# Kernel tuning notes

Measured on AMD Instinct MI355X. Metric: run time of the kernel, lower is better.

## Reference

```python
import jax, jax.numpy as jnp
import numpy as np

D_MODEL = 512
D_STATE = 128
D_CONV = 4
EXPAND = 2
HEADDIM = 64
NLAYERS = 2
D_INNER = EXPAND * D_MODEL          # 1024
NHEADS = D_INNER // HEADDIM         # 16
CONV_DIM = D_INNER + 2 * D_STATE    # 1280 (x, B, C share the depthwise conv)
D_IN_PROJ = 2 * D_INNER + 2 * D_STATE + NHEADS  # 2320 (z, xBC, dt)
VOCAB = 40
SEQ = 64
BATCH = 512
NUM_CLASSES = 2
FC_HID = 128
EPS = 1e-5


def setup_inputs() -> dict:
    key = jax.random.key(0)
    ks = jax.random.split(key, 12)
    x = jax.random.randint(ks[0], (BATCH, SEQ), 0, VOCAB)
    emb = jax.random.uniform(ks[1], (VOCAB, D_MODEL), minval=-0.1, maxval=0.1)
    emb = emb.at[0].set(0.0)  # padding_idx=0
    pos = jax.random.normal(ks[2], (1, SEQ, D_MODEL)) * 0.02
    in_proj_w = jax.random.normal(ks[3], (NLAYERS, D_IN_PROJ, D_MODEL)) * 0.02
    conv_w = jax.random.normal(ks[4], (NLAYERS, CONV_DIM, D_CONV)) * 0.1
    conv_b = jnp.zeros((NLAYERS, CONV_DIM))
    dt0 = jax.random.uniform(ks[5], (NLAYERS, NHEADS), minval=1e-3, maxval=0.1)
    dt_bias = dt0 + jnp.log(-jnp.expm1(-dt0))  # inverse softplus of dt0
    A_log = jnp.log(jax.random.uniform(ks[6], (NLAYERS, NHEADS), minval=1.0, maxval=16.0))
    D_skip = jnp.ones((NLAYERS, NHEADS))
    norm_w = jnp.ones((NLAYERS, D_INNER))
    out_proj_w = jax.random.normal(ks[7], (NLAYERS, D_MODEL, D_INNER)) * 0.02
    ln_g = jnp.ones((NLAYERS, D_MODEL))
    ln_b = jnp.zeros((NLAYERS, D_MODEL))
    fc1_w = jax.random.uniform(ks[8], (FC_HID, D_MODEL), minval=-0.1, maxval=0.1)
    fc1_b = jnp.zeros((FC_HID,))
    fc2_w = jax.random.uniform(ks[9], (NUM_CLASSES, FC_HID), minval=-0.1, maxval=0.1)
    fc2_b = jnp.zeros((NUM_CLASSES,))
    return dict(x=x, emb=emb, pos=pos, in_proj_w=in_proj_w, conv_w=conv_w,
                conv_b=conv_b, dt_bias=dt_bias, A_log=A_log, D_skip=D_skip,
                norm_w=norm_w, out_proj_w=out_proj_w, ln_g=ln_g, ln_b=ln_b,
                fc1_w=fc1_w, fc1_b=fc1_b, fc2_w=fc2_w, fc2_b=fc2_b)


def _layernorm(h, g, b):
    mu = jnp.mean(h, axis=-1, keepdims=True)
    var = jnp.mean(jnp.square(h - mu), axis=-1, keepdims=True)
    return (h - mu) * jax.lax.rsqrt(var + EPS) * g + b


def _mamba2_block(h, in_proj_w, conv_w, conv_b, dt_bias, A_log, D_skip, norm_w, out_proj_w):
    b, s, _ = h.shape
    zxbcdt = jnp.einsum('bsd,ed->bse', h, in_proj_w)  # [b,s,D_IN_PROJ]
    z = zxbcdt[..., :D_INNER]
    xBC = zxbcdt[..., D_INNER:D_INNER + CONV_DIM]
    dt_raw = zxbcdt[..., D_INNER + CONV_DIM:]          # [b,s,NHEADS]
    # causal depthwise 1D conv + silu
    xBC_t = jnp.pad(jnp.swapaxes(xBC, 1, 2), ((0, 0), (0, 0), (D_CONV - 1, 0)))
    conv = jax.lax.conv_general_dilated(xBC_t, conv_w[:, None, :], (1,), 'VALID',
                                        feature_group_count=CONV_DIM)
    xBC = jax.nn.silu(jnp.swapaxes(conv + conv_b[None, :, None], 1, 2))
    xs = xBC[..., :D_INNER].reshape(b, s, NHEADS, HEADDIM)
    Bm = xBC[..., D_INNER:D_INNER + D_STATE]           # [b,s,n] (ngroups=1)
    Cm = xBC[..., D_INNER + D_STATE:]                  # [b,s,n]
    dt = jax.nn.softplus(dt_raw + dt_bias)             # [b,s,h]
    A = -jnp.exp(A_log)                                # [h], negative
    # exact quadratic (1-semiseparable) SSD form, equal to the selective scan
    cum = jnp.cumsum(dt * A, axis=1)                   # [b,s,h]
    diff = cum[:, :, None, :] - cum[:, None, :, :]     # [b,i,j,h] <= 0 for i>=j
    causal = jnp.tril(jnp.ones((s, s), dtype=bool))
    L = jnp.exp(jnp.where(causal[None, :, :, None], diff, -jnp.inf))  # decay mask
    scores = jnp.einsum('bin,bjn->bij', Cm, Bm)
    M = scores[..., None] * L                          # [b,i,j,h]
    y = jnp.einsum('bijh,bjh,bjhp->bihp', M, dt, xs)
    y = y + D_skip[None, None, :, None] * xs
    y = y.reshape(b, s, D_INNER)
    # gated RMSNorm
    y = y * jax.nn.silu(z)
    y = y * jax.lax.rsqrt(jnp.mean(jnp.square(y), axis=-1, keepdims=True) + EPS) * norm_w
    return jnp.einsum('bsi,di->bsd', y, out_proj_w)


def reference(x, emb, pos, in_proj_w, conv_w, conv_b, dt_bias, A_log, D_skip,
              norm_w, out_proj_w, ln_g, ln_b, fc1_w, fc1_b, fc2_w, fc2_b):
    h = emb[x] + pos[:, :x.shape[1], :]  # dropout is identity in eval
    for l in range(NLAYERS):
        y = _mamba2_block(h, in_proj_w[l], conv_w[l], conv_b[l], dt_bias[l],
                          A_log[l], D_skip[l], norm_w[l], out_proj_w[l])
        h = h + _layernorm(y, ln_g[l], ln_b[l])
    pm = (jnp.sum(h, axis=-1) != 0).astype(h.dtype)[..., None]  # [b,s,1]
    pooled = jnp.sum(h * pm, axis=1) / jnp.clip(jnp.sum(pm, axis=1), 1.0, None)
    hid = jax.nn.relu(pooled @ fc1_w.T + fc1_b)
    return hid @ fc2_w.T + fc2_b
```

## Files before the change

kernel.cpp:

```cpp
#include <hip/hip_runtime.h>
#include <hip/hip_bf16.h>

#define D_MODEL   512
#define D_STATE   128
#define D_CONV    4
#define HEADDIM   64
#define NLAYERS   2
#define D_INNER   1024
#define NHEADS    16
#define CONV_DIM  1280
#define D_IN_PROJ 2320
#define NPAD      2432
#define SEQ       64
#define BATCH     512
#define NTOK      (BATCH*SEQ)
#define FC_HID    128
#define EPS       1e-5f

using bf16 = __hip_bfloat16;
typedef __bf16 bf16x8 __attribute__((ext_vector_type(8)));
typedef float  f32x4  __attribute__((ext_vector_type(4)));

__device__ __forceinline__ float b2f(bf16 v)  { return __bfloat162float(v); }
__device__ __forceinline__ bf16  f2b(float v) { return __float2bfloat16(v); }
__device__ __forceinline__ float bflo(unsigned u){ return __builtin_bit_cast(float, u << 16); }
__device__ __forceinline__ float bfhi(unsigned u){ return __builtin_bit_cast(float, u & 0xffff0000u); }

__device__ __forceinline__ void gl_lds16(const void* g, void* l) {
    __builtin_amdgcn_global_load_lds((const __attribute__((address_space(1))) void*)g,
                                     (__attribute__((address_space(3))) void*)l, 16, 0, 0);
}

__global__ __launch_bounds__(256) void k_embed(const int* __restrict__ x,
        const float* __restrict__ emb, const float* __restrict__ pos,
        float* __restrict__ h, bf16* __restrict__ hb) {
    int idx = blockIdx.x*256 + threadIdx.x;
    int d   = idx & (D_MODEL-1);
    int tok = idx >> 9;
    int s   = tok & (SEQ-1);
    int v   = x[tok];
    float r = emb[v*D_MODEL + d] + pos[s*D_MODEL + d];
    h[idx]  = r;
    hb[idx] = f2b(r);
}

__global__ __launch_bounds__(256) void k_cvtw(const float* __restrict__ src,
        bf16* __restrict__ dst, int R, int Kc, int total8) {
    int idx = blockIdx.x*256 + threadIdx.x;
    if (idx >= total8) return;
    int e0 = idx*8;
    int r = e0 / Kc, c = e0 % Kc;
    bf16 tb[8];
    if (r < R) {
        float4 f0 = *(const float4*)(src + (size_t)r*Kc + c);
        float4 f1 = *(const float4*)(src + (size_t)r*Kc + c + 4);
        tb[0]=f2b(f0.x); tb[1]=f2b(f0.y); tb[2]=f2b(f0.z); tb[3]=f2b(f0.w);
        tb[4]=f2b(f1.x); tb[5]=f2b(f1.y); tb[6]=f2b(f1.z); tb[7]=f2b(f1.w);
    } else {
        #pragma unroll
        for (int e=0;e<8;e++) tb[e] = f2b(0.f);
    }
    *(uint4*)(dst + (size_t)r*Kc + c) = *(uint4*)&tb[0];
}

template<int FUSE, int KDIM>
__global__ __launch_bounds__(256) void k_gemm128(const bf16* __restrict__ A,
        const bf16* __restrict__ B, bf16* __restrict__ C,
        bf16* __restrict__ xbcc, float* __restrict__ dt, float* __restrict__ cum,
        const float* __restrict__ cw, const float* __restrict__ cb,
        const float* __restrict__ dt_bias, const float* __restrict__ A_log,
        int Nout, int nbx, int ctok)
{
    constexpr int NT = KDIM / 64;
    __shared__ __align__(16) char lds[65536];
    bf16* Cs = (bf16*)lds;

    const int nwg = gridDim.x;
    const int q = nwg >> 3, r = nwg & 7;
    const int xcd = blockIdx.x & 7, loc = blockIdx.x >> 3;
    const int wg = ((xcd < r) ? xcd*(q+1) : r*(q+1) + (xcd-r)*q) + loc;
    const int m0 = (wg / nbx) * 128;
    const int n0 = (wg % nbx) * 128;

    const int t = threadIdx.x;
    const int wid = t >> 6, lane = t & 63;
    const int lr = lane & 15, lg = lane >> 4;
    const int wm = (wid >> 1)*64, wn = (wid & 1)*64;
    const int srow = wid*32;
    const int sr   = lane >> 3;
    const int scol = ((lane & 7) ^ sr) * 8;

    const bf16* Abase = A + (size_t)(m0 + srow + sr)*KDIM + scol;
    const bf16* Bbase = B + (size_t)(n0 + srow + sr)*KDIM + scol;

    f32x4 acc[4][4] = {};
    char* bc = lds;
    char* bn = lds + 32768;

    auto STAGE = [&](char* buf, int kk) {
        #pragma unroll
        for (int c = 0; c < 4; c++) {
            gl_lds16(Abase + (size_t)(c*8)*KDIM + kk, buf + (srow + c*8)*128);
            gl_lds16(Bbase + (size_t)(c*8)*KDIM + kk, buf + 16384 + (srow + c*8)*128);
        }
    };

    STAGE(bc, 0);
    asm volatile("s_waitcnt vmcnt(0)" ::: "memory");
    __builtin_amdgcn_s_barrier();

    #pragma unroll
    for (int kt = 0; kt < NT; kt++) {
        if (kt + 1 < NT) STAGE(bn, (kt+1)*64);
        #pragma unroll
        for (int ks = 0; ks < 64; ks += 32) {
            bf16x8 a[4], b[4];
            #pragma unroll
            for (int mi=0;mi<4;mi++) {
                int ra = wm + mi*16 + lr;
                a[mi] = *(const bf16x8*)(bc + ra*128 + ((((ks>>3)+lg) ^ (ra&7))<<4));
            }
            #pragma unroll
            for (int ni=0;ni<4;ni++) {
                int rb = wn + ni*16 + lr;
                b[ni] = *(const bf16x8*)(bc + 16384 + rb*128 + ((((ks>>3)+lg) ^ (rb&7))<<4));
            }
            __builtin_amdgcn_s_setprio(1);
            #pragma unroll
            for (int mi=0;mi<4;mi++)
                #pragma unroll
                for (int ni=0;ni<4;ni++)
                    acc[mi][ni] = __builtin_amdgcn_mfma_f32_16x16x32_bf16(a[mi], b[ni], acc[mi][ni], 0,0,0);
            __builtin_amdgcn_s_setprio(0);
        }
        asm volatile("s_waitcnt vmcnt(0)" ::: "memory");
        __builtin_amdgcn_s_barrier();
        char* tb2 = bc; bc = bn; bn = tb2;
    }
    __builtin_amdgcn_sched_barrier(0);

    #pragma unroll
    for (int mi=0;mi<4;mi++)
        #pragma unroll
        for (int ni=0;ni<4;ni++)
            #pragma unroll
            for (int rr=0;rr<4;rr++)
                Cs[(wm+mi*16+lg*4+rr)*136 + wn+ni*16+lr] = f2b(acc[mi][ni][rr]);
    __syncthreads();

    const int rsub = t >> 4;
    const int c8   = (t & 15) * 8;

    if (FUSE == 0 || n0 < 1024) {
        const int strd = (FUSE == 0) ? Nout : 1024;
        #pragma unroll
        for (int it = 0; it < 8; it++) {
            int row = it*16 + rsub;
            int gcol = n0 + c8;
            if (FUSE == 0 && gcol >= Nout) continue;
            *(uint4*)(C + (size_t)(m0+row)*strd + gcol) = *(const uint4*)&Cs[row*136 + c8];
        }
    } else if (n0 < 2304) {
        const int cbase = n0 - 1024 + c8;
        float4 wreg[8]; float bias[8];
        #pragma unroll
        for (int e=0;e<8;e++) wreg[e] = *(const float4*)(cw + (size_t)(cbase+e)*4);
        {
            float4 b0 = *(const float4*)(cb + cbase);
            float4 b1 = *(const float4*)(cb + cbase + 4);
            bias[0]=b0.x; bias[1]=b0.y; bias[2]=b0.z; bias[3]=b0.w;
            bias[4]=b1.x; bias[5]=b1.y; bias[6]=b1.z; bias[7]=b1.w;
        }
        #pragma unroll
        for (int it = 0; it < 8; it++) {
            int row = it*16 + rsub;
            int sl  = row & (SEQ-1);
            float m3 = (sl >= 3) ? 1.f : 0.f;
            float m2 = (sl >= 2) ? 1.f : 0.f;
            float m1 = (sl >= 1) ? 1.f : 0.f;
            const bf16* sm3 = &Cs[(row-3)*136 + c8];
            const bf16* sm2 = &Cs[(row-2)*136 + c8];
            const bf16* sm1 = &Cs[(row-1)*136 + c8];
            const bf16* sm0 = &Cs[(row  )*136 + c8];
            float a[8];
            #pragma unroll
            for (int e=0;e<8;e++) {
                a[e] = bias[e]
                     + m3 * b2f(sm3[e]) * wreg[e].x
                     + m2 * b2f(sm2[e]) * wreg[e].y
                     + m1 * b2f(sm1[e]) * wreg[e].z
                     +      b2f(sm0[e]) * wreg[e].w;
            }
            bf16 outv[8];
            #pragma unroll
            for (int e=0;e<8;e++) outv[e] = f2b(a[e] / (1.f + __expf(-a[e])));
            *(uint4*)(xbcc + (size_t)(m0+row)*CONV_DIM + cbase) = *(uint4*)&outv[0];
        }
    } else {
        for (int p = wid; p < 32; p += 4) {
            int sq = p >> 4, head = p & 15;
            float raw = b2f(Cs[(sq*64 + lane)*136 + head]) + dt_bias[head];
            float dval = (raw > 20.f) ? raw : log1pf(__expf(raw));
            float Ah = -__expf(A_log[head]);
            float cc = dval * Ah;
            #pragma unroll
            for (int o=1;o<64;o<<=1) { float v = __shfl_up(cc, o); if (lane >= o) cc += v; }
            int tok = m0 + sq*64 + lane;
            dt [(size_t)head*ctok + tok] = dval;
            cum[(size_t)head*ctok + tok] = cc;
        }
    }
}

__global__ __launch_bounds__(256) void k_ssd(const bf16* __restrict__ xbcc,
        const float* __restrict__ dt, const float* __restrict__ cum,
        const float* __restrict__ Dskip, bf16* __restrict__ y, int ctok) {
    __shared__ float scores[64][66];
    __shared__ __align__(16) bf16 Wb [64][72];
    __shared__ __align__(16) bf16 xsT[64][72];
    __shared__ __align__(16) bf16 ys [64][72];
    const int bid = blockIdx.x;
    const int b   = bid >> 1;
    const int hg  = (bid & 1) * 8;
    const int t = threadIdx.x;
    const size_t tokbase = (size_t)b*SEQ;
    const int lane = t & 63, lr = lane & 15, lg = lane >> 4;
    const int w = t >> 6;

    {
        int i0 = w*16;
        f32x4 sacc[4] = {};
        const bf16* Cbase = xbcc + tokbase*CONV_DIM + D_INNER + D_STATE;
        const bf16* Bbase = xbcc + tokbase*CONV_DIM + D_INNER;
        #pragma unroll
        for (int ks = 0; ks < D_STATE; ks += 32) {
            bf16x8 af = *(const bf16x8*)(Cbase + (size_t)(i0+lr)*CONV_DIM + ks + lg*8);
            #pragma unroll
            for (int jt = 0; jt < 4; jt++) {
                bf16x8 bfr = *(const bf16x8*)(Bbase + (size_t)(jt*16+lr)*CONV_DIM + ks + lg*8);
                sacc[jt] = __builtin_amdgcn_mfma_f32_16x16x32_bf16(af, bfr, sacc[jt], 0,0,0);
            }
        }
        #pragma unroll
        for (int jt=0;jt<4;jt++)
            #pragma unroll
            for (int rr=0;rr<4;rr++)
                scores[i0 + lg*4 + rr][jt*16 + lr] = sacc[jt][rr];
    }

    const int wi = t >> 2;
    const int wj0 = (t & 3) * 16;

    for (int hl = 0; hl < 8; hl++) {
        const int hh = hg + hl;
        const size_t cbase = (size_t)hh*ctok + tokbase;
        __syncthreads();

        #pragma unroll
        for (int cc = 0; cc < 2; cc++) {
            int ch = cc*256 + t;
            int rr = ch >> 3, c8 = (ch & 7)*8;
            uint4 v = *(const uint4*)(xbcc + (tokbase + rr)*CONV_DIM + hh*HEADDIM + c8);
            const bf16* pv = (const bf16*)&v;
            #pragma unroll
            for (int e=0;e<8;e++) xsT[c8+e][rr] = pv[e];
        }
        {
            float cum_i = cum[cbase + wi];
            float cjf[16], djf[16];
            #pragma unroll
            for (int qq=0; qq<4; qq++) {
                float4 a4 = *(const float4*)(cum + cbase + wj0 + qq*4);
                float4 d4 = *(const float4*)(dt  + cbase + wj0 + qq*4);
                cjf[qq*4+0]=a4.x; cjf[qq*4+1]=a4.y; cjf[qq*4+2]=a4.z; cjf[qq*4+3]=a4.w;
                djf[qq*4+0]=d4.x; djf[qq*4+1]=d4.y; djf[qq*4+2]=d4.z; djf[qq*4+3]=d4.w;
            }
            bf16 tb[16];
            #pragma unroll
            for (int e=0;e<16;e++) {
                int j = wj0 + e;
                float wv = (j <= wi) ? scores[wi][j] * __expf(cum_i - cjf[e]) * djf[e] : 0.f;
                tb[e] = f2b(wv);
            }
            *(uint4*)&Wb[wi][wj0]   = *(uint4*)&tb[0];
            *(uint4*)&Wb[wi][wj0+8] = *(uint4*)&tb[8];
        }
        __syncthreads();

        {
            float dsk = Dskip[hh];
            f32x4 yacc[4] = {};
            #pragma unroll
            for (int ks = 0; ks < 64; ks += 32) {
                bf16x8 a = *(const bf16x8*)&Wb[w*16 + lr][ks + lg*8];
                #pragma unroll
                for (int n=0; n<4; n++) {
                    bf16x8 bb = *(const bf16x8*)&xsT[n*16 + lr][ks + lg*8];
                    yacc[n] = __builtin_amdgcn_mfma_f32_16x16x32_bf16(a, bb, yacc[n], 0,0,0);
                }
            }
            #pragma unroll
            for (int n=0; n<4; n++)
                #pragma unroll
                for (int rr=0; rr<4; rr++) {
                    int row = w*16 + lg*4 + rr;
                    int col = n*16 + lr;
                    ys[row][col] = f2b(yacc[n][rr] + dsk * b2f(xsT[col][row]));
                }
        }
        __syncthreads();

        #pragma unroll
        for (int cc = 0; cc < 2; cc++) {
            int ch = cc*256 + t;
            int rr = ch >> 3, c8 = (ch & 7)*8;
            *(uint4*)(y + (tokbase + rr)*D_INNER + hh*HEADDIM + c8) = *(const uint4*)&ys[rr][c8];
        }
    }
}

__global__ __launch_bounds__(256) void k_gaterms(bf16* __restrict__ y,
        const bf16* __restrict__ zbuf, const float* __restrict__ nw) {
    int tok = blockIdx.x, t = threadIdx.x;
    __shared__ float red[4];
    int d = t*4;
    uint2 yv = *(const uint2*)(y    + (size_t)tok*D_INNER + d);
    uint2 zv = *(const uint2*)(zbuf + (size_t)tok*D_INNER + d);
    const unsigned* yu = (const unsigned*)&yv;
    const unsigned* zu = (const unsigned*)&zv;
    float g[4]; float ss = 0.f;
    #pragma unroll
    for (int e=0;e<2;e++) {
        float y0 = bflo(yu[e]), y1 = bfhi(yu[e]);
        float z0 = bflo(zu[e]), z1 = bfhi(zu[e]);
        float g0 = y0 * z0 / (1.f + __expf(-z0));
        float g1 = y1 * z1 / (1.f + __expf(-z1));
        g[2*e] = g0; g[2*e+1] = g1;
        ss += g0*g0 + g1*g1;
    }
    for (int o=32;o>0;o>>=1) ss += __shfl_down(ss, o);
    if ((t & 63) == 0) red[t>>6] = ss;
    __syncthreads();
    float tot = red[0]+red[1]+red[2]+red[3];
    float scale = rsqrtf(tot/(float)D_INNER + EPS);
    bf16 outv[4];
    #pragma unroll
    for (int e=0;e<4;e++) outv[e] = f2b(g[e] * scale * nw[d+e]);
    *(uint2*)(y + (size_t)tok*D_INNER + d) = *(uint2*)&outv[0];
}

__global__ __launch_bounds__(256) void k_resln(float* __restrict__ h,
        bf16* __restrict__ hb, const bf16* __restrict__ tmp,
        const float* __restrict__ g, const float* __restrict__ bb) {
    int tok = blockIdx.x, t = threadIdx.x;
    __shared__ float redS[4], redQ[4];
    int d = t*2;
    unsigned u = *(const unsigned*)(tmp + (size_t)tok*D_MODEL + d);
    float v0 = bflo(u), v1 = bfhi(u);
    float s = v0+v1, q = v0*v0+v1*v1;
    for (int o=32;o>0;o>>=1){ s += __shfl_down(s,o); q += __shfl_down(q,o); }
    if ((t&63)==0){ redS[t>>6]=s; redQ[t>>6]=q; }
    __syncthreads();
    float S = redS[0]+redS[1]+redS[2]+redS[3];
    float Q = redQ[0]+redQ[1]+redQ[2]+redQ[3];
    float mu  = S/(float)D_MODEL;
    float var = Q/(float)D_MODEL - mu*mu;
    float inv = rsqrtf(var + EPS);
    size_t base = (size_t)tok*D_MODEL + d;
    float h0 = h[base]   + (v0-mu)*inv*g[d]   + bb[d];
    float h1 = h[base+1] + (v1-mu)*inv*g[d+1] + bb[d+1];
    h[base] = h0; h[base+1] = h1;
    bf16 o2[2] = { f2b(h0), f2b(h1) };
    *(unsigned*)(hb + base) = *(unsigned*)&o2[0];
}

__global__ __launch_bounds__(256) void k_pool(const float* __restrict__ h,
        float* __restrict__ pooled) {
    int b = blockIdx.x, t = threadIdx.x;
    __shared__ float ps[64][4];
    __shared__ float pm[64];
    __shared__ float cntS;
    {
        int s = t >> 2, q = t & 3;
        const float4* row = (const float4*)(h + ((size_t)b*SEQ + s)*D_MODEL + q*128);
        float acc = 0;
        #pragma unroll 8
        for (int e=0;e<32;e++) { float4 f = row[e]; acc += f.x+f.y+f.z+f.w; }
        ps[s][q] = acc;
    }
    __syncthreads();
    if (t < 64) pm[t] = (ps[t][0]+ps[t][1]+ps[t][2]+ps[t][3]) != 0.f ? 1.f : 0.f;
    __syncthreads();
    if (t == 0) { float c=0; for (int s2=0;s2<64;s2++) c+=pm[s2]; cntS = fmaxf(c,1.f); }
    __syncthreads();
    float cnt = cntS;
    #pragma unroll
    for (int rep=0;rep<2;rep++) {
        int d = t + rep*256;
        float acc = 0;
        for (int s2=0;s2<64;s2++) acc += h[((size_t)b*SEQ+s2)*D_MODEL + d] * pm[s2];
        pooled[(size_t)b*D_MODEL + d] = acc / cnt;
    }
}

__global__ __launch_bounds__(128) void k_fc(const float* __restrict__ pooled,
        const float* __restrict__ w1, const float* __restrict__ b1,
        const float* __restrict__ w2, const float* __restrict__ b2,
        float* __restrict__ out) {
    int b = blockIdx.x, j = threadIdx.x;
    __shared__ float hid[FC_HID];
    const float* p  = pooled + (size_t)b*D_MODEL;
    const float* wr = w1 + (size_t)j*D_MODEL;
    float acc = b1[j];
    for (int d=0; d<D_MODEL; d+=4)
        acc += p[d]*wr[d] + p[d+1]*wr[d+1] + p[d+2]*wr[d+2] + p[d+3]*wr[d+3];
    hid[j] = fmaxf(acc, 0.f);
    __syncthreads();
    if (j < 2) {
        float o = b2[j];
        for (int k=0;k<FC_HID;k++) o += hid[k]*w2[j*FC_HID+k];
        out[b*2 + j] = o;
    }
}

extern "C" void kernel_launch(void* const* d_in, const int* in_sizes, int n_in,
                              void* d_out, int out_size, void* d_ws, size_t ws_size,
                              hipStream_t stream) {
    (void)in_sizes; (void)n_in; (void)out_size;
    const int*   x        = (const int*)  d_in[0];
    const float* emb      = (const float*)d_in[1];
    const float* pos      = (const float*)d_in[2];
    const float* in_proj  = (const float*)d_in[3];
    const float* conv_w   = (const float*)d_in[4];
    const float* conv_b   = (const float*)d_in[5];
    const float* dt_bias  = (const float*)d_in[6];
    const float* A_log    = (const float*)d_in[7];
    const float* D_skip   = (const float*)d_in[8];
    const float* norm_w   = (const float*)d_in[9];
    const float* out_proj = (const float*)d_in[10];
    const float* ln_g     = (const float*)d_in[11];
    const float* ln_b     = (const float*)d_in[12];
    const float* fc1_w    = (const float*)d_in[13];
    const float* fc1_b    = (const float*)d_in[14];
    const float* fc2_w    = (const float*)d_in[15];
    const float* fc2_b    = (const float*)d_in[16];
    float* out = (float*)d_out;

    const size_t H_B   = (size_t)NTOK * D_MODEL * 4;
    const size_t HB_B  = (size_t)NTOK * D_MODEL * 2;
    const size_t WPI_B = (size_t)NPAD * D_MODEL * 2;
    const size_t WPO_B = (size_t)D_MODEL * D_INNER * 2;
    const size_t PBASE = H_B + HB_B + NLAYERS*(WPI_B + WPO_B);

    const size_t PER_TOK = 2048 + 2560 + 2048 + 128;
    int CB = BATCH;
    while (CB > 8 && PBASE + (size_t)CB*SEQ*PER_TOK > ws_size) CB >>= 1;
    const int CT = CB * SEQ;
    const int NC = BATCH / CB;

    char* ws = (char*)d_ws;
    float* h    = (float*)(ws);
    bf16*  hb   = (bf16*) (ws + H_B);
    bf16*  wpi  = (bf16*) (ws + H_B + HB_B);
    bf16*  wpo  = (bf16*) (ws + H_B + HB_B + NLAYERS*WPI_B);
    char*  tr   = ws + PBASE;
    bf16*  zbuf = (bf16*) (tr);
    bf16*  xbcc = (bf16*) (tr + (size_t)CT*2048);
    bf16*  ybuf = (bf16*) (tr + (size_t)CT*(2048+2560));
    float* dt   = (float*)(tr + (size_t)CT*(2048+2560+2048));
    float* cum  = dt + (size_t)CT*NHEADS;
    bf16*  tmp  = xbcc;
    float* pooled = (float*)tr;

    for (int l = 0; l < NLAYERS; l++) {
        int t8i = NPAD*D_MODEL/8;
        k_cvtw<<<(t8i+255)/256, 256, 0, stream>>>(in_proj + (size_t)l*D_IN_PROJ*D_MODEL,
                wpi + (size_t)l*NPAD*D_MODEL, D_IN_PROJ, D_MODEL, t8i);
        int t8o = D_MODEL*D_INNER/8;
        k_cvtw<<<(t8o+255)/256, 256, 0, stream>>>(out_proj + (size_t)l*D_MODEL*D_INNER,
                wpo + (size_t)l*D_MODEL*D_INNER, D_MODEL, D_INNER, t8o);
    }

    k_embed<<<(NTOK*D_MODEL)/256, 256, 0, stream>>>(x, emb, pos, h, hb);

    const int NBX_I = NPAD/128;
    const int NBX_O = D_MODEL/128;

    for (int l = 0; l < NLAYERS; l++) {
        const bf16* wi = wpi + (size_t)l*NPAD*D_MODEL;
        const bf16* wo = wpo + (size_t)l*D_MODEL*D_INNER;
        for (int c = 0; c < NC; c++) {
            const int tok0 = c * CT;
            float* hc  = h  + (size_t)tok0 * D_MODEL;
            bf16*  hbc = hb + (size_t)tok0 * D_MODEL;
            k_gemm128<1,512><<<(CT/128)*NBX_I, 256, 0, stream>>>(hbc, wi, zbuf,
                    xbcc, dt, cum,
                    conv_w + (size_t)l*CONV_DIM*D_CONV, conv_b + (size_t)l*CONV_DIM,
                    dt_bias + l*NHEADS, A_log + l*NHEADS,
                    NPAD, NBX_I, CT);
            k_ssd<<<CB*2, 256, 0, stream>>>(xbcc, dt, cum, D_skip + l*NHEADS, ybuf, CT);
            k_gaterms<<<CT, 256, 0, stream>>>(ybuf, zbuf, norm_w + (size_t)l*D_INNER);
            k_gemm128<0,1024><<<(CT/128)*NBX_O, 256, 0, stream>>>(ybuf, wo, tmp,
                    nullptr, nullptr, nullptr, nullptr, nullptr, nullptr, nullptr,
                    D_MODEL, NBX_O, CT);
            k_resln<<<CT, 256, 0, stream>>>(hc, hbc, tmp, ln_g + l*D_MODEL, ln_b + l*D_MODEL);
        }
    }

    k_pool<<<BATCH, 256, 0, stream>>>(h, pooled);
    k_fc<<<BATCH, FC_HID, 0, stream>>>(pooled, fc1_w, fc1_b, fc2_w, fc2_b, out);
}
```

Baseline: 667.2 us.

## Use 256x256 in-projection GEMM tile and vectorize elementwise kernels

Replaces the fused in-projection GEMM with a 256x256-tile, 512-thread kernel that uses 128KB of dynamic LDS and pads N to 2560. The fused conv/SiLU and dt/cumsum epilogue now runs in two 128-row halves. The embed, gated-RMSNorm and residual-LayerNorm kernels are widened to handle more elements per thread and two tokens per block. This aims to raise MFMA data reuse and cut per-block overhead, at the cost of more padded columns, lower occupancy from the large LDS footprint and higher register pressure.

```diff
diff --git a/kernel.cpp b/kernel.cpp
--- a/kernel.cpp
+++ b/kernel.cpp
@@ -10,7 +10,7 @@
 #define NHEADS    16
 #define CONV_DIM  1280
 #define D_IN_PROJ 2320
-#define NPAD      2432
+#define NPAD      2560
 #define SEQ       64
 #define BATCH     512
 #define NTOK      (BATCH*SEQ)
@@ -35,13 +35,16 @@
         const float* __restrict__ emb, const float* __restrict__ pos,
         float* __restrict__ h, bf16* __restrict__ hb) {
     int idx = blockIdx.x*256 + threadIdx.x;
-    int d   = idx & (D_MODEL-1);
-    int tok = idx >> 9;
+    int d   = (idx & 127) * 4;
+    int tok = idx >> 7;
     int s   = tok & (SEQ-1);
     int v   = x[tok];
-    float r = emb[v*D_MODEL + d] + pos[s*D_MODEL + d];
-    h[idx]  = r;
-    hb[idx] = f2b(r);
+    float4 e4 = *(const float4*)(emb + (size_t)v*D_MODEL + d);
+    float4 p4 = *(const float4*)(pos + (size_t)s*D_MODEL + d);
+    float4 r; r.x=e4.x+p4.x; r.y=e4.y+p4.y; r.z=e4.z+p4.z; r.w=e4.w+p4.w;
+    *(float4*)(h + (size_t)tok*D_MODEL + d) = r;
+    bf16 o[4] = { f2b(r.x), f2b(r.y), f2b(r.z), f2b(r.w) };
+    *(uint2*)(hb + (size_t)tok*D_MODEL + d) = *(uint2*)&o[0];
 }
 
 __global__ __launch_bounds__(256) void k_cvtw(const float* __restrict__ src,
@@ -63,15 +66,162 @@
     *(uint4*)(dst + (size_t)r*Kc + c) = *(uint4*)&tb[0];
 }
 
-template<int FUSE, int KDIM>
-__global__ __launch_bounds__(256) void k_gemm128(const bf16* __restrict__ A,
-        const bf16* __restrict__ B, bf16* __restrict__ C,
+__global__ __launch_bounds__(512) void k_gemm256(const bf16* __restrict__ A,
+        const bf16* __restrict__ B, bf16* __restrict__ zbuf,
         bf16* __restrict__ xbcc, float* __restrict__ dt, float* __restrict__ cum,
         const float* __restrict__ cw, const float* __restrict__ cb,
         const float* __restrict__ dt_bias, const float* __restrict__ A_log,
-        int Nout, int nbx, int ctok)
+        int ctok)
 {
-    constexpr int NT = KDIM / 64;
+    constexpr int KDIM = 512, NT = KDIM/64, NBX = NPAD/256;
+    extern __shared__ __align__(16) char lds[];
+    bf16* Cs = (bf16*)lds;
+
+    const int nwg = gridDim.x;
+    const int q = nwg >> 3, r = nwg & 7;
+    const int xcd = blockIdx.x & 7, loc = blockIdx.x >> 3;
+    const int wg = ((xcd < r) ? xcd*(q+1) : r*(q+1) + (xcd-r)*q) + loc;
+    const int m0 = (wg / NBX) * 256;
+    const int n0 = (wg % NBX) * 256;
+
+    const int t = threadIdx.x;
+    const int wid = t >> 6, lane = t & 63;
+    const int lr = lane & 15, lg = lane >> 4;
+    const int wm = (wid >> 2)*128, wn = (wid & 3)*64;
+    const int srow = wid*32;
+    const int sr   = lane >> 3;
+    const int scol = ((lane & 7) ^ sr) * 8;
+
+    const bf16* Abase = A + (size_t)(m0 + srow + sr)*KDIM + scol;
+    const bf16* Bbase = B + (size_t)(n0 + srow + sr)*KDIM + scol;
+
+    f32x4 acc[8][4] = {};
+    char* bc = lds;
+    char* bn = lds + 65536;
+
+    auto STAGE = [&](char* buf, int kk) {
+        #pragma unroll
+        for (int c = 0; c < 4; c++) {
+            gl_lds16(Abase + (size_t)(c*8)*KDIM + kk, buf + (srow + c*8)*128);
+            gl_lds16(Bbase + (size_t)(c*8)*KDIM + kk, buf + 32768 + (srow + c*8)*128);
+        }
+    };
+
+    STAGE(bc, 0);
+    asm volatile("s_waitcnt vmcnt(0)" ::: "memory");
+    __builtin_amdgcn_s_barrier();
+
+    #pragma unroll
+    for (int kt = 0; kt < NT; kt++) {
+        if (kt + 1 < NT) STAGE(bn, (kt+1)*64);
+        #pragma unroll
+        for (int ks = 0; ks < 64; ks += 32) {
+            bf16x8 a[8], b[4];
+            #pragma unroll
+            for (int mi=0;mi<8;mi++) {
+                int ra = wm + mi*16 + lr;
+                a[mi] = *(const bf16x8*)(bc + ra*128 + ((((ks>>3)+lg) ^ (ra&7))<<4));
+            }
+            #pragma unroll
+            for (int ni=0;ni<4;ni++) {
+                int rb = wn + ni*16 + lr;
+                b[ni] = *(const bf16x8*)(bc + 32768 + rb*128 + ((((ks>>3)+lg) ^ (rb&7))<<4));
+            }
+            __builtin_amdgcn_s_setprio(1);
+            #pragma unroll
+            for (int mi=0;mi<8;mi++)
+                #pragma unroll
+                for (int ni=0;ni<4;ni++)
+                    acc[mi][ni] = __builtin_amdgcn_mfma_f32_16x16x32_bf16(a[mi], b[ni], acc[mi][ni], 0,0,0);
+            __builtin_amdgcn_s_setprio(0);
+        }
+        asm volatile("s_waitcnt vmcnt(0)" ::: "memory");
+        __builtin_amdgcn_s_barrier();
+        char* tb2 = bc; bc = bn; bn = tb2;
+    }
+    __builtin_amdgcn_sched_barrier(0);
+
+    const int myhalf = wid >> 2;
+    const int rsub = t >> 5;
+    const int c8   = (t & 31) * 8;
+
+    for (int hp = 0; hp < 2; hp++) {
+        __syncthreads();
+        if (myhalf == hp) {
+            #pragma unroll
+            for (int mi=0;mi<8;mi++)
+                #pragma unroll
+                for (int ni=0;ni<4;ni++)
+                    #pragma unroll
+                    for (int rr=0;rr<4;rr++)
+                        Cs[(mi*16+lg*4+rr)*264 + wn+ni*16+lr] = f2b(acc[mi][ni][rr]);
+        }
+        __syncthreads();
+        const int R0 = hp*128;
+
+        if (n0 < 1024) {
+            #pragma unroll
+            for (int it = 0; it < 8; it++) {
+                int row = it*16 + rsub;
+                *(uint4*)(zbuf + (size_t)(m0+R0+row)*1024 + n0 + c8) = *(const uint4*)&Cs[row*264 + c8];
+            }
+        } else if (n0 < 2304) {
+            const int cbase = n0 - 1024 + c8;
+            float4 wreg[8]; float bias[8];
+            #pragma unroll
+            for (int e=0;e<8;e++) wreg[e] = *(const float4*)(cw + (size_t)(cbase+e)*4);
+            {
+                float4 b0 = *(const float4*)(cb + cbase);
+                float4 b1 = *(const float4*)(cb + cbase + 4);
+                bias[0]=b0.x; bias[1]=b0.y; bias[2]=b0.z; bias[3]=b0.w;
+                bias[4]=b1.x; bias[5]=b1.y; bias[6]=b1.z; bias[7]=b1.w;
+            }
+            #pragma unroll
+            for (int it = 0; it < 8; it++) {
+                int row = it*16 + rsub;
+                int sl  = row & (SEQ-1);
+                float m3 = (sl >= 3) ? 1.f : 0.f;
+                float m2 = (sl >= 2) ? 1.f : 0.f;
+                float m1 = (sl >= 1) ? 1.f : 0.f;
+                const bf16* sm3 = &Cs[(row-3)*264 + c8];
+                const bf16* sm2 = &Cs[(row-2)*264 + c8];
+                const bf16* sm1 = &Cs[(row-1)*264 + c8];
+                const bf16* sm0 = &Cs[(row  )*264 + c8];
+                float a[8];
+                #pragma unroll
+                for (int e=0;e<8;e++) {
+                    a[e] = bias[e]
+                         + m3 * b2f(sm3[e]) * wreg[e].x
+                         + m2 * b2f(sm2[e]) * wreg[e].y
+                         + m1 * b2f(sm1[e]) * wreg[e].z
+                         +      b2f(sm0[e]) * wreg[e].w;
+                }
+                bf16 outv[8];
+                #pragma unroll
+                for (int e=0;e<8;e++) outv[e] = f2b(a[e] / (1.f + __expf(-a[e])));
+                *(uint4*)(xbcc + (size_t)(m0+R0+row)*CONV_DIM + cbase) = *(uint4*)&outv[0];
+            }
+        } else {
+            for (int p = wid; p < 32; p += 8) {
+                int sq = p >> 4, head = p & 15;
+                float raw = b2f(Cs[(sq*64 + lane)*264 + head]) + dt_bias[head];
+                float dval = (raw > 20.f) ? raw : log1pf(__expf(raw));
+                float Ah = -__expf(A_log[head]);
+                float cc = dval * Ah;
+                #pragma unroll
+                for (int o=1;o<64;o<<=1) { float v = __shfl_up(cc, o); if (lane >= o) cc += v; }
+                int tok = m0 + R0 + sq*64 + lane;
+                dt [(size_t)head*ctok + tok] = dval;
+                cum[(size_t)head*ctok + tok] = cc;
+            }
+        }
+    }
+}
+
+__global__ __launch_bounds__(256) void k_gemm128(const bf16* __restrict__ A,
+        const bf16* __restrict__ B, bf16* __restrict__ C, int Nout, int nbx)
+{
+    constexpr int KDIM = 1024, NT = KDIM/64;
     __shared__ __align__(16) char lds[65536];
     bf16* Cs = (bf16*)lds;
 
@@ -147,68 +297,12 @@
             for (int rr=0;rr<4;rr++)
                 Cs[(wm+mi*16+lg*4+rr)*136 + wn+ni*16+lr] = f2b(acc[mi][ni][rr]);
     __syncthreads();
-
     const int rsub = t >> 4;
     const int c8   = (t & 15) * 8;
-
-    if (FUSE == 0 || n0 < 1024) {
-        const int strd = (FUSE == 0) ? Nout : 1024;
-        #pragma unroll
-        for (int it = 0; it < 8; it++) {
-            int row = it*16 + rsub;
-            int gcol = n0 + c8;
-            if (FUSE == 0 && gcol >= Nout) continue;
-            *(uint4*)(C + (size_t)(m0+row)*strd + gcol) = *(const uint4*)&Cs[row*136 + c8];
-        }
-    } else if (n0 < 2304) {
-        const int cbase = n0 - 1024 + c8;
-        float4 wreg[8]; float bias[8];
-        #pragma unroll
-        for (int e=0;e<8;e++) wreg[e] = *(const float4*)(cw + (size_t)(cbase+e)*4);
-        {
-            float4 b0 = *(const float4*)(cb + cbase);
-            float4 b1 = *(const float4*)(cb + cbase + 4);
-            bias[0]=b0.x; bias[1]=b0.y; bias[2]=b0.z; bias[3]=b0.w;
-            bias[4]=b1.x; bias[5]=b1.y; bias[6]=b1.z; bias[7]=b1.w;
-        }
-        #pragma unroll
-        for (int it = 0; it < 8; it++) {
-            int row = it*16 + rsub;
-            int sl  = row & (SEQ-1);
-            float m3 = (sl >= 3) ? 1.f : 0.f;
-            float m2 = (sl >= 2) ? 1.f : 0.f;
-            float m1 = (sl >= 1) ? 1.f : 0.f;
-            const bf16* sm3 = &Cs[(row-3)*136 + c8];
-            const bf16* sm2 = &Cs[(row-2)*136 + c8];
-            const bf16* sm1 = &Cs[(row-1)*136 + c8];
-            const bf16* sm0 = &Cs[(row  )*136 + c8];
-            float a[8];
-            #pragma unroll
-            for (int e=0;e<8;e++) {
-                a[e] = bias[e]
-                     + m3 * b2f(sm3[e]) * wreg[e].x
-                     + m2 * b2f(sm2[e]) * wreg[e].y
-                     + m1 * b2f(sm1[e]) * wreg[e].z
-                     +      b2f(sm0[e]) * wreg[e].w;
-            }
-            bf16 outv[8];
-            #pragma unroll
-            for (int e=0;e<8;e++) outv[e] = f2b(a[e] / (1.f + __expf(-a[e])));
-            *(uint4*)(xbcc + (size_t)(m0+row)*CONV_DIM + cbase) = *(uint4*)&outv[0];
-        }
-    } else {
-        for (int p = wid; p < 32; p += 4) {
-            int sq = p >> 4, head = p & 15;
-            float raw = b2f(Cs[(sq*64 + lane)*136 + head]) + dt_bias[head];
-            float dval = (raw > 20.f) ? raw : log1pf(__expf(raw));
-            float Ah = -__expf(A_log[head]);
-            float cc = dval * Ah;
-            #pragma unroll
-            for (int o=1;o<64;o<<=1) { float v = __shfl_up(cc, o); if (lane >= o) cc += v; }
-            int tok = m0 + sq*64 + lane;
-            dt [(size_t)head*ctok + tok] = dval;
-            cum[(size_t)head*ctok + tok] = cc;
-        }
+    #pragma unroll
+    for (int it = 0; it < 8; it++) {
+        int row = it*16 + rsub;
+        *(uint4*)(C + (size_t)(m0+row)*Nout + n0 + c8) = *(const uint4*)&Cs[row*136 + c8];
     }
 }
 
@@ -321,16 +415,18 @@
 
 __global__ __launch_bounds__(256) void k_gaterms(bf16* __restrict__ y,
         const bf16* __restrict__ zbuf, const float* __restrict__ nw) {
-    int tok = blockIdx.x, t = threadIdx.x;
-    __shared__ float red[4];
-    int d = t*4;
-    uint2 yv = *(const uint2*)(y    + (size_t)tok*D_INNER + d);
-    uint2 zv = *(const uint2*)(zbuf + (size_t)tok*D_INNER + d);
+    int tok = blockIdx.x*2 + (threadIdx.x >> 7);
+    int t   = threadIdx.x & 127;
+    int hi  = threadIdx.x >> 7, wv = (threadIdx.x >> 6) & 1;
+    __shared__ float red[2][2];
+    int d = t*8;
+    uint4 yv = *(const uint4*)(y    + (size_t)tok*D_INNER + d);
+    uint4 zv = *(const uint4*)(zbuf + (size_t)tok*D_INNER + d);
     const unsigned* yu = (const unsigned*)&yv;
     const unsigned* zu = (const unsigned*)&zv;
-    float g[4]; float ss = 0.f;
+    float g[8]; float ss = 0.f;
     #pragma unroll
-    for (int e=0;e<2;e++) {
+    for (int e=0;e<4;e++) {
         float y0 = bflo(yu[e]), y1 = bfhi(yu[e]);
         float z0 = bflo(zu[e]), z1 = bfhi(zu[e]);
         float g0 = y0 * z0 / (1.f + __expf(-z0));
@@ -339,39 +435,47 @@
         ss += g0*g0 + g1*g1;
     }
     for (int o=32;o>0;o>>=1) ss += __shfl_down(ss, o);
-    if ((t & 63) == 0) red[t>>6] = ss;
+    if ((threadIdx.x & 63) == 0) red[hi][wv] = ss;
     __syncthreads();
-    float tot = red[0]+red[1]+red[2]+red[3];
-    float scale = rsqrtf(tot/(float)D_INNER + EPS);
-    bf16 outv[4];
+    float scale = rsqrtf((red[hi][0]+red[hi][1])/(float)D_INNER + EPS);
+    bf16 outv[8];
     #pragma unroll
-    for (int e=0;e<4;e++) outv[e] = f2b(g[e] * scale * nw[d+e]);
-    *(uint2*)(y + (size_t)tok*D_INNER + d) = *(uint2*)&outv[0];
+    for (int e=0;e<8;e++) outv[e] = f2b(g[e] * scale * nw[d+e]);
+    *(uint4*)(y + (size_t)tok*D_INNER + d) = *(uint4*)&outv[0];
 }
 
 __global__ __launch_bounds__(256) void k_resln(float* __restrict__ h,
         bf16* __restrict__ hb, const bf16* __restrict__ tmp,
         const float* __restrict__ g, const float* __restrict__ bb) {
-    int tok = blockIdx.x, t = threadIdx.x;
-    __shared__ float redS[4], redQ[4];
-    int d = t*2;
-    unsigned u = *(const unsigned*)(tmp + (size_t)tok*D_MODEL + d);
-    float v0 = bflo(u), v1 = bfhi(u);
-    float s = v0+v1, q = v0*v0+v1*v1;
-    for (int o=32;o>0;o>>=1){ s += __shfl_down(s,o); q += __shfl_down(q,o); }
-    if ((t&63)==0){ redS[t>>6]=s; redQ[t>>6]=q; }
+    int tok = blockIdx.x*2 + (threadIdx.x >> 7);
+    int t   = threadIdx.x & 127;
+    int hi  = threadIdx.x >> 7, wv = (threadIdx.x >> 6) & 1;
+    __shared__ float redS[2][2], redQ[2][2];
+    int d = t*4;
+    uint2 u2 = *(const uint2*)(tmp + (size_t)tok*D_MODEL + d);
+    const unsigned* uu = (const unsigned*)&u2;
+    float v0 = bflo(uu[0]), v1 = bfhi(uu[0]), v2 = bflo(uu[1]), v3 = bfhi(uu[1]);
+    float s = v0+v1+v2+v3;
+    float qq = v0*v0+v1*v1+v2*v2+v3*v3;
+    for (int o=32;o>0;o>>=1){ s += __shfl_down(s,o); qq += __shfl_down(qq,o); }
+    if ((threadIdx.x & 63) == 0){ redS[hi][wv]=s; redQ[hi][wv]=qq; }
     __syncthreads();
-    float S = redS[0]+redS[1]+redS[2]+redS[3];
-    float Q = redQ[0]+redQ[1]+redQ[2]+redQ[3];
+    float S = redS[hi][0]+redS[hi][1];
+    float Q = redQ[hi][0]+redQ[hi][1];
     float mu  = S/(float)D_MODEL;
     float var = Q/(float)D_MODEL - mu*mu;
     float inv = rsqrtf(var + EPS);
     size_t base = (size_t)tok*D_MODEL + d;
-    float h0 = h[base]   + (v0-mu)*inv*g[d]   + bb[d];
-    float h1 = h[base+1] + (v1-mu)*inv*g[d+1] + bb[d+1];
-    h[base] = h0; h[base+1] = h1;
-    bf16 o2[2] = { f2b(h0), f2b(h1) };
-    *(unsigned*)(hb + base) = *(unsigned*)&o2[0];
+    float4 h4 = *(const float4*)(h + base);
+    float4 g4 = *(const float4*)(g + d);
+    float4 b4 = *(const float4*)(bb + d);
+    h4.x += (v0-mu)*inv*g4.x + b4.x;
+    h4.y += (v1-mu)*inv*g4.y + b4.y;
+    h4.z += (v2-mu)*inv*g4.z + b4.z;
+    h4.w += (v3-mu)*inv*g4.w + b4.w;
+    *(float4*)(h + base) = h4;
+    bf16 o4[4] = { f2b(h4.x), f2b(h4.y), f2b(h4.z), f2b(h4.w) };
+    *(uint2*)(hb + base) = *(uint2*)&o4[0];
 }
 
 __global__ __launch_bounds__(256) void k_pool(const float* __restrict__ h,
@@ -381,12 +485,12 @@
     __shared__ float pm[64];
     __shared__ float cntS;
     {
-        int s = t >> 2, q = t & 3;
-        const float4* row = (const float4*)(h + ((size_t)b*SEQ + s)*D_MODEL + q*128);
+        int s = t >> 2, qq = t & 3;
+        const float4* row = (const float4*)(h + ((size_t)b*SEQ + s)*D_MODEL + qq*128);
         float acc = 0;
         #pragma unroll 8
         for (int e=0;e<32;e++) { float4 f = row[e]; acc += f.x+f.y+f.z+f.w; }
-        ps[s][q] = acc;
+        ps[s][qq] = acc;
     }
     __syncthreads();
     if (t < 64) pm[t] = (ps[t][0]+ps[t][1]+ps[t][2]+ps[t][3]) != 0.f ? 1.f : 0.f;
@@ -446,6 +550,9 @@
     const float* fc2_b    = (const float*)d_in[16];
     float* out = (float*)d_out;
 
+    (void)hipFuncSetAttribute((const void*)k_gemm256,
+            hipFuncAttributeMaxDynamicSharedMemorySize, 131072);
+
     const size_t H_B   = (size_t)NTOK * D_MODEL * 4;
     const size_t HB_B  = (size_t)NTOK * D_MODEL * 2;
     const size_t WPI_B = (size_t)NPAD * D_MODEL * 2;
@@ -481,9 +588,8 @@
                 wpo + (size_t)l*D_MODEL*D_INNER, D_MODEL, D_INNER, t8o);
     }
 
-    k_embed<<<(NTOK*D_MODEL)/256, 256, 0, stream>>>(x, emb, pos, h, hb);
-
-    const int NBX_I = NPAD/128;
+    k_embed<<<(NTOK*128)/256, 256, 0, stream>>>(x, emb, pos, h, hb);
+
     const int NBX_O = D_MODEL/128;
 
     for (int l = 0; l < NLAYERS; l++) {
@@ -493,17 +599,14 @@
             const int tok0 = c * CT;
             float* hc  = h  + (size_t)tok0 * D_MODEL;
             bf16*  hbc = hb + (size_t)tok0 * D_MODEL;
-            k_gemm128<1,512><<<(CT/128)*NBX_I, 256, 0, stream>>>(hbc, wi, zbuf,
+            k_gemm256<<<(CT/256)*(NPAD/256), 512, 131072, stream>>>(hbc, wi, zbuf,
                     xbcc, dt, cum,
                     conv_w + (size_t)l*CONV_DIM*D_CONV, conv_b + (size_t)l*CONV_DIM,
-                    dt_bias + l*NHEADS, A_log + l*NHEADS,
-                    NPAD, NBX_I, CT);
+                    dt_bias + l*NHEADS, A_log + l*NHEADS, CT);
             k_ssd<<<CB*2, 256, 0, stream>>>(xbcc, dt, cum, D_skip + l*NHEADS, ybuf, CT);
-            k_gaterms<<<CT, 256, 0, stream>>>(ybuf, zbuf, norm_w + (size_t)l*D_INNER);
-            k_gemm128<0,1024><<<(CT/128)*NBX_O, 256, 0, stream>>>(ybuf, wo, tmp,
-                    nullptr, nullptr, nullptr, nullptr, nullptr, nullptr, nullptr,
-                    D_MODEL, NBX_O, CT);
-            k_resln<<<CT, 256, 0, stream>>>(hc, hbc, tmp, ln_g + l*D_MODEL, ln_b + l*D_MODEL);
+            k_gaterms<<<CT/2, 256, 0, stream>>>(ybuf, zbuf, norm_w + (size_t)l*D_INNER);
+            k_gemm128<<<(CT/128)*NBX_O, 256, 0, stream>>>(ybuf, wo, tmp, D_MODEL, NBX_O);
+            k_resln<<<CT/2, 256, 0, stream>>>(hc, hbc, tmp, ln_g + l*D_MODEL, ln_b + l*D_MODEL);
         }
     }
 
```

Result: slower. 808.2 us (+21.1%).

## Single-buffer GEMM LDS with swizzled epilogue and vectorize elementwise kernels

Applied to the files above, without the earlier changes.

The GEMM drops its double-buffered LDS prefetch for a single 32KB buffer with plain __syncthreads, which halves LDS use and may allow more resident workgroups. The output staging tile moves from padded rows to an XOR-swizzled layout. The embed, gated RMSNorm and residual LayerNorm kernels are widened to 16-byte/float4 accesses, and the norm kernels now process two tokens per block. The single-buffer GEMM loses the overlap of global loads with MFMA compute and the priority hints, so it risks more stalls.

```diff
diff --git a/kernel.cpp b/kernel.cpp
--- a/kernel.cpp
+++ b/kernel.cpp
@@ -35,13 +35,16 @@
         const float* __restrict__ emb, const float* __restrict__ pos,
         float* __restrict__ h, bf16* __restrict__ hb) {
     int idx = blockIdx.x*256 + threadIdx.x;
-    int d   = idx & (D_MODEL-1);
-    int tok = idx >> 9;
+    int d   = (idx & 127) * 4;
+    int tok = idx >> 7;
     int s   = tok & (SEQ-1);
     int v   = x[tok];
-    float r = emb[v*D_MODEL + d] + pos[s*D_MODEL + d];
-    h[idx]  = r;
-    hb[idx] = f2b(r);
+    float4 e4 = *(const float4*)(emb + (size_t)v*D_MODEL + d);
+    float4 p4 = *(const float4*)(pos + (size_t)s*D_MODEL + d);
+    float4 r; r.x=e4.x+p4.x; r.y=e4.y+p4.y; r.z=e4.z+p4.z; r.w=e4.w+p4.w;
+    *(float4*)(h + (size_t)tok*D_MODEL + d) = r;
+    bf16 o[4] = { f2b(r.x), f2b(r.y), f2b(r.z), f2b(r.w) };
+    *(uint2*)(hb + (size_t)tok*D_MODEL + d) = *(uint2*)&o[0];
 }
 
 __global__ __launch_bounds__(256) void k_cvtw(const float* __restrict__ src,
@@ -72,7 +75,7 @@
         int Nout, int nbx, int ctok)
 {
     constexpr int NT = KDIM / 64;
-    __shared__ __align__(16) char lds[65536];
+    __shared__ __align__(16) char lds[32768];
     bf16* Cs = (bf16*)lds;
 
     const int nwg = gridDim.x;
@@ -94,58 +97,47 @@
     const bf16* Bbase = B + (size_t)(n0 + srow + sr)*KDIM + scol;
 
     f32x4 acc[4][4] = {};
-    char* bc = lds;
-    char* bn = lds + 32768;
-
-    auto STAGE = [&](char* buf, int kk) {
+
+    for (int kt = 0; kt < NT; kt++) {
+        const int kk = kt*64;
         #pragma unroll
         for (int c = 0; c < 4; c++) {
-            gl_lds16(Abase + (size_t)(c*8)*KDIM + kk, buf + (srow + c*8)*128);
-            gl_lds16(Bbase + (size_t)(c*8)*KDIM + kk, buf + 16384 + (srow + c*8)*128);
-        }
-    };
-
-    STAGE(bc, 0);
-    asm volatile("s_waitcnt vmcnt(0)" ::: "memory");
-    __builtin_amdgcn_s_barrier();
-
-    #pragma unroll
-    for (int kt = 0; kt < NT; kt++) {
-        if (kt + 1 < NT) STAGE(bn, (kt+1)*64);
+            gl_lds16(Abase + (size_t)(c*8)*KDIM + kk, lds + (srow + c*8)*128);
+            gl_lds16(Bbase + (size_t)(c*8)*KDIM + kk, lds + 16384 + (srow + c*8)*128);
+        }
+        __syncthreads();
         #pragma unroll
         for (int ks = 0; ks < 64; ks += 32) {
             bf16x8 a[4], b[4];
             #pragma unroll
             for (int mi=0;mi<4;mi++) {
                 int ra = wm + mi*16 + lr;
-                a[mi] = *(const bf16x8*)(bc + ra*128 + ((((ks>>3)+lg) ^ (ra&7))<<4));
+                a[mi] = *(const bf16x8*)(lds + ra*128 + ((((ks>>3)+lg) ^ (ra&7))<<4));
             }
             #pragma unroll
             for (int ni=0;ni<4;ni++) {
                 int rb = wn + ni*16 + lr;
-                b[ni] = *(const bf16x8*)(bc + 16384 + rb*128 + ((((ks>>3)+lg) ^ (rb&7))<<4));
-            }
-            __builtin_amdgcn_s_setprio(1);
+                b[ni] = *(const bf16x8*)(lds + 16384 + rb*128 + ((((ks>>3)+lg) ^ (rb&7))<<4));
+            }
             #pragma unroll
             for (int mi=0;mi<4;mi++)
                 #pragma unroll
                 for (int ni=0;ni<4;ni++)
                     acc[mi][ni] = __builtin_amdgcn_mfma_f32_16x16x32_bf16(a[mi], b[ni], acc[mi][ni], 0,0,0);
-            __builtin_amdgcn_s_setprio(0);
-        }
-        asm volatile("s_waitcnt vmcnt(0)" ::: "memory");
-        __builtin_amdgcn_s_barrier();
-        char* tb2 = bc; bc = bn; bn = tb2;
-    }
-    __builtin_amdgcn_sched_barrier(0);
+        }
+        __syncthreads();
+    }
 
     #pragma unroll
     for (int mi=0;mi<4;mi++)
         #pragma unroll
         for (int ni=0;ni<4;ni++)
             #pragma unroll
-            for (int rr=0;rr<4;rr++)
-                Cs[(wm+mi*16+lg*4+rr)*136 + wn+ni*16+lr] = f2b(acc[mi][ni][rr]);
+            for (int rr=0;rr<4;rr++) {
+                int row = wm + mi*16 + lg*4 + rr;
+                int col = (wn + ni*16 + lr) ^ ((row & 7) << 3);
+                Cs[row*128 + col] = f2b(acc[mi][ni][rr]);
+            }
     __syncthreads();
 
     const int rsub = t >> 4;
@@ -156,9 +148,8 @@
         #pragma unroll
         for (int it = 0; it < 8; it++) {
             int row = it*16 + rsub;
-            int gcol = n0 + c8;
-            if (FUSE == 0 && gcol >= Nout) continue;
-            *(uint4*)(C + (size_t)(m0+row)*strd + gcol) = *(const uint4*)&Cs[row*136 + c8];
+            const bf16* src = &Cs[row*128 + (c8 ^ ((row & 7) << 3))];
+            *(uint4*)(C + (size_t)(m0+row)*strd + n0 + c8) = *(const uint4*)src;
         }
     } else if (n0 < 2304) {
         const int cbase = n0 - 1024 + c8;
@@ -178,10 +169,10 @@
             float m3 = (sl >= 3) ? 1.f : 0.f;
             float m2 = (sl >= 2) ? 1.f : 0.f;
             float m1 = (sl >= 1) ? 1.f : 0.f;
-            const bf16* sm3 = &Cs[(row-3)*136 + c8];
-            const bf16* sm2 = &Cs[(row-2)*136 + c8];
-            const bf16* sm1 = &Cs[(row-1)*136 + c8];
-            const bf16* sm0 = &Cs[(row  )*136 + c8];
+            const bf16* sm3 = &Cs[(row-3)*128 + (c8 ^ (((row-3) & 7) << 3))];
+            const bf16* sm2 = &Cs[(row-2)*128 + (c8 ^ (((row-2) & 7) << 3))];
+            const bf16* sm1 = &Cs[(row-1)*128 + (c8 ^ (((row-1) & 7) << 3))];
+            const bf16* sm0 = &Cs[(row  )*128 + (c8 ^ (((row  ) & 7) << 3))];
             float a[8];
             #pragma unroll
             for (int e=0;e<8;e++) {
@@ -199,13 +190,14 @@
     } else {
         for (int p = wid; p < 32; p += 4) {
             int sq = p >> 4, head = p & 15;
-            float raw = b2f(Cs[(sq*64 + lane)*136 + head]) + dt_bias[head];
+            int row = sq*64 + lane;
+            float raw = b2f(Cs[row*128 + (head ^ ((row & 7) << 3))]) + dt_bias[head];
             float dval = (raw > 20.f) ? raw : log1pf(__expf(raw));
             float Ah = -__expf(A_log[head]);
             float cc = dval * Ah;
             #pragma unroll
             for (int o=1;o<64;o<<=1) { float v = __shfl_up(cc, o); if (lane >= o) cc += v; }
-            int tok = m0 + sq*64 + lane;
+            int tok = m0 + row;
             dt [(size_t)head*ctok + tok] = dval;
             cum[(size_t)head*ctok + tok] = cc;
         }
@@ -321,16 +313,18 @@
 
 __global__ __launch_bounds__(256) void k_gaterms(bf16* __restrict__ y,
         const bf16* __restrict__ zbuf, const float* __restrict__ nw) {
-    int tok = blockIdx.x, t = threadIdx.x;
-    __shared__ float red[4];
-    int d = t*4;
-    uint2 yv = *(const uint2*)(y    + (size_t)tok*D_INNER + d);
-    uint2 zv = *(const uint2*)(zbuf + (size_t)tok*D_INNER + d);
+    int tok = blockIdx.x*2 + (threadIdx.x >> 7);
+    int t   = threadIdx.x & 127;
+    int hi  = threadIdx.x >> 7, wv = (threadIdx.x >> 6) & 1;
+    __shared__ float red[2][2];
+    int d = t*8;
+    uint4 yv = *(const uint4*)(y    + (size_t)tok*D_INNER + d);
+    uint4 zv = *(const uint4*)(zbuf + (size_t)tok*D_INNER + d);
     const unsigned* yu = (const unsigned*)&yv;
     const unsigned* zu = (const unsigned*)&zv;
-    float g[4]; float ss = 0.f;
+    float g[8]; float ss = 0.f;
     #pragma unroll
-    for (int e=0;e<2;e++) {
+    for (int e=0;e<4;e++) {
         float y0 = bflo(yu[e]), y1 = bfhi(yu[e]);
         float z0 = bflo(zu[e]), z1 = bfhi(zu[e]);
         float g0 = y0 * z0 / (1.f + __expf(-z0));
@@ -339,39 +333,47 @@
         ss += g0*g0 + g1*g1;
     }
     for (int o=32;o>0;o>>=1) ss += __shfl_down(ss, o);
-    if ((t & 63) == 0) red[t>>6] = ss;
-    __syncthreads();
-    float tot = red[0]+red[1]+red[2]+red[3];
-    float scale = rsqrtf(tot/(float)D_INNER + EPS);
-    bf16 outv[4];
+    if ((threadIdx.x & 63) == 0) red[hi][wv] = ss;
+    __syncthreads();
+    float scale = rsqrtf((red[hi][0]+red[hi][1])/(float)D_INNER + EPS);
+    bf16 outv[8];
     #pragma unroll
-    for (int e=0;e<4;e++) outv[e] = f2b(g[e] * scale * nw[d+e]);
-    *(uint2*)(y + (size_t)tok*D_INNER + d) = *(uint2*)&outv[0];
+    for (int e=0;e<8;e++) outv[e] = f2b(g[e] * scale * nw[d+e]);
+    *(uint4*)(y + (size_t)tok*D_INNER + d) = *(uint4*)&outv[0];
 }
 
 __global__ __launch_bounds__(256) void k_resln(float* __restrict__ h,
         bf16* __restrict__ hb, const bf16* __restrict__ tmp,
         const float* __restrict__ g, const float* __restrict__ bb) {
-    int tok = blockIdx.x, t = threadIdx.x;
-    __shared__ float redS[4], redQ[4];
-    int d = t*2;
-    unsigned u = *(const unsigned*)(tmp + (size_t)tok*D_MODEL + d);
-    float v0 = bflo(u), v1 = bfhi(u);
-    float s = v0+v1, q = v0*v0+v1*v1;
-    for (int o=32;o>0;o>>=1){ s += __shfl_down(s,o); q += __shfl_down(q,o); }
-    if ((t&63)==0){ redS[t>>6]=s; redQ[t>>6]=q; }
-    __syncthreads();
-    float S = redS[0]+redS[1]+redS[2]+redS[3];
-    float Q = redQ[0]+redQ[1]+redQ[2]+redQ[3];
+    int tok = blockIdx.x*2 + (threadIdx.x >> 7);
+    int t   = threadIdx.x & 127;
+    int hi  = threadIdx.x >> 7, wv = (threadIdx.x >> 6) & 1;
+    __shared__ float redS[2][2], redQ[2][2];
+    int d = t*4;
+    uint2 u2 = *(const uint2*)(tmp + (size_t)tok*D_MODEL + d);
+    const unsigned* uu = (const unsigned*)&u2;
+    float v0 = bflo(uu[0]), v1 = bfhi(uu[0]), v2 = bflo(uu[1]), v3 = bfhi(uu[1]);
+    float s = v0+v1+v2+v3;
+    float qq = v0*v0+v1*v1+v2*v2+v3*v3;
+    for (int o=32;o>0;o>>=1){ s += __shfl_down(s,o); qq += __shfl_down(qq,o); }
+    if ((threadIdx.x & 63) == 0){ redS[hi][wv]=s; redQ[hi][wv]=qq; }
+    __syncthreads();
+    float S = redS[hi][0]+redS[hi][1];
+    float Q = redQ[hi][0]+redQ[hi][1];
     float mu  = S/(float)D_MODEL;
     float var = Q/(float)D_MODEL - mu*mu;
     float inv = rsqrtf(var + EPS);
     size_t base = (size_t)tok*D_MODEL + d;
-    float h0 = h[base]   + (v0-mu)*inv*g[d]   + bb[d];
-    float h1 = h[base+1] + (v1-mu)*inv*g[d+1] + bb[d+1];
-    h[base] = h0; h[base+1] = h1;
-    bf16 o2[2] = { f2b(h0), f2b(h1) };
-    *(unsigned*)(hb + base) = *(unsigned*)&o2[0];
+    float4 h4 = *(const float4*)(h + base);
+    float4 g4 = *(const float4*)(g + d);
+    float4 b4 = *(const float4*)(bb + d);
+    h4.x += (v0-mu)*inv*g4.x + b4.x;
+    h4.y += (v1-mu)*inv*g4.y + b4.y;
+    h4.z += (v2-mu)*inv*g4.z + b4.z;
+    h4.w += (v3-mu)*inv*g4.w + b4.w;
+    *(float4*)(h + base) = h4;
+    bf16 o4[4] = { f2b(h4.x), f2b(h4.y), f2b(h4.z), f2b(h4.w) };
+    *(uint2*)(hb + base) = *(uint2*)&o4[0];
 }
 
 __global__ __launch_bounds__(256) void k_pool(const float* __restrict__ h,
@@ -381,12 +383,12 @@
     __shared__ float pm[64];
     __shared__ float cntS;
     {
-        int s = t >> 2, q = t & 3;
-        const float4* row = (const float4*)(h + ((size_t)b*SEQ + s)*D_MODEL + q*128);
+        int s = t >> 2, qq = t & 3;
+        const float4* row = (const float4*)(h + ((size_t)b*SEQ + s)*D_MODEL + qq*128);
         float acc = 0;
         #pragma unroll 8
         for (int e=0;e<32;e++) { float4 f = row[e]; acc += f.x+f.y+f.z+f.w; }
-        ps[s][q] = acc;
+        ps[s][qq] = acc;
     }
     __syncthreads();
     if (t < 64) pm[t] = (ps[t][0]+ps[t][1]+ps[t][2]+ps[t][3]) != 0.f ? 1.f : 0.f;
@@ -481,7 +483,7 @@
                 wpo + (size_t)l*D_MODEL*D_INNER, D_MODEL, D_INNER, t8o);
     }
 
-    k_embed<<<(NTOK*D_MODEL)/256, 256, 0, stream>>>(x, emb, pos, h, hb);
+    k_embed<<<(NTOK*128)/256, 256, 0, stream>>>(x, emb, pos, h, hb);
 
     const int NBX_I = NPAD/128;
     const int NBX_O = D_MODEL/128;
@@ -499,11 +501,11 @@
                     dt_bias + l*NHEADS, A_log + l*NHEADS,
                     NPAD, NBX_I, CT);
             k_ssd<<<CB*2, 256, 0, stream>>>(xbcc, dt, cum, D_skip + l*NHEADS, ybuf, CT);
-            k_gaterms<<<CT, 256, 0, stream>>>(ybuf, zbuf, norm_w + (size_t)l*D_INNER);
+            k_gaterms<<<CT/2, 256, 0, stream>>>(ybuf, zbuf, norm_w + (size_t)l*D_INNER);
             k_gemm128<0,1024><<<(CT/128)*NBX_O, 256, 0, stream>>>(ybuf, wo, tmp,
                     nullptr, nullptr, nullptr, nullptr, nullptr, nullptr, nullptr,
                     D_MODEL, NBX_O, CT);
-            k_resln<<<CT, 256, 0, stream>>>(hc, hbc, tmp, ln_g + l*D_MODEL, ln_b + l*D_MODEL);
+            k_resln<<<CT/2, 256, 0, stream>>>(hc, hbc, tmp, ln_g + l*D_MODEL, ln_b + l*D_MODEL);
         }
     }
 
```

Measured after the change: 719.9 us. 1.08x slower.
